# Optimization experiments

Hardware: AMD Instinct MI355X
Metric: run time of the kernel (lower is better)

The kernel has to match this reference:

```python
import jax, jax.numpy as jnp
import numpy as np

B, H, E, G, SEQ_LEN = 131072, 64, 16, 32, 30


def setup_inputs() -> dict:
    key = jax.random.key(0)
    ks = jax.random.split(key, 17)
    def lin(kw, kb, out_f, in_f):
        s = 1.0 / np.sqrt(in_f)
        W = jax.random.uniform(kw, (out_f, in_f), jnp.float32, -s, s)
        b = jax.random.uniform(kb, (out_f,), jnp.float32, -s, s)
        return W, b
    W_se, b_se = lin(ks[0], ks[1], E, 2)
    W_h2p, b_h2p = lin(ks[2], ks[3], 2, 3 * H)
    W_goal, b_goal = lin(ks[4], ks[5], H, 2 * G)
    W_abs, b_abs = lin(ks[6], ks[7], H, 2)
    W_ih, b_ih = lin(ks[8], ks[9], 4 * H, E)
    W_hh, b_hh = lin(ks[10], ks[11], 4 * H, H)
    return {
        "traj_abs": jax.random.normal(ks[12], (1, B, 2), jnp.float32),
        "traj_rel": jax.random.normal(ks[13], (1, B, 2), jnp.float32),
        "h0": jax.random.normal(ks[14], (1, B, H), jnp.float32),
        "c0": jax.random.normal(ks[15], (1, B, H), jnp.float32),
        "goals": jax.random.normal(ks[16], (B, G, 2), jnp.float32),
        "W_ih": W_ih, "W_hh": W_hh, "b_ih": b_ih, "b_hh": b_hh,
        "W_se": W_se, "b_se": b_se,
        "W_h2p": W_h2p, "b_h2p": b_h2p,
        "W_goal": W_goal, "b_goal": b_goal,
        "W_abs": W_abs, "b_abs": b_abs,
    }


def reference(traj_abs, traj_rel, h0, c0, goals,
              W_ih, W_hh, b_ih, b_hh,
              W_se, b_se, W_h2p, b_h2p,
              W_goal, b_goal, W_abs, b_abs):
    b = traj_abs.shape[1]
    goal_emb = goals.reshape(b, -1) @ W_goal.T + b_goal            # (b, H)
    dec_in = jax.nn.leaky_relu(traj_rel[0] @ W_se.T + b_se)        # (b, E)

    def step(carry, _):
        h, c, x, abs_pos = carry
        gates = x @ W_ih.T + b_ih + h @ W_hh.T + b_hh              # (b, 4H)
        i, f, g, o = jnp.split(gates, 4, axis=-1)                  # PyTorch gate order
        c = jax.nn.sigmoid(f) * c + jax.nn.sigmoid(i) * jnp.tanh(g)
        h = jax.nn.sigmoid(o) * jnp.tanh(c)
        abs_emb = abs_pos @ W_abs.T + b_abs                        # (b, H)
        inp = jnp.concatenate([h, abs_emb, goal_emb], axis=1)      # (b, 3H)
        rel = inp @ W_h2p.T + b_h2p                                # (b, 2)
        x = jax.nn.leaky_relu(rel @ W_se.T + b_se)
        return (h, c, x, abs_pos + rel), rel

    _, rels = jax.lax.scan(step, (h0[0], c0[0], dec_in, traj_abs[0]),
                           None, length=SEQ_LEN)
    return rels  # (seq_len, b, 2)
```

## Files before the change

### kernel.cpp

```cpp
#include <hip/hip_runtime.h>
#include <stdint.h>


#define B_TOT 131072
#define SEQL 30
#define NT 4

typedef _Float16 f16x8 __attribute__((ext_vector_type(8)));
typedef _Float16 f16x2 __attribute__((ext_vector_type(2)));
typedef float f32x4 __attribute__((ext_vector_type(4)));
typedef float f32x2 __attribute__((ext_vector_type(2)));

__device__ __forceinline__ float fexp2(float x) {
#if __has_builtin(__builtin_amdgcn_exp2f)
  return __builtin_amdgcn_exp2f(x);
#else
  return exp2f(x);
#endif
}
__device__ __forceinline__ float frcp(float x) {
#if __has_builtin(__builtin_amdgcn_rcpf)
  return __builtin_amdgcn_rcpf(x);
#else
  return 1.0f / x;
#endif
}

__global__ void setup_consts(const float* __restrict__ Wgoal,
                             const float* __restrict__ bgoal,
                             const float* __restrict__ Wh2p,
                             const float* __restrict__ bh2p,
                             const float* __restrict__ Wabs,
                             const float* __restrict__ babs,
                             float* __restrict__ wsf) {
  const int tid = threadIdx.x;
  const int wv = tid >> 6;
  const int lane = tid & 63;
  if (wv == 0) {
    const int k = lane;
    float s0 = 0.f, s1 = 0.f;
#pragma unroll 8
    for (int jj = 0; jj < 64; ++jj) {
      float wg = Wgoal[jj * 64 + k];
      s0 += wg * Wh2p[128 + jj];
      s1 += wg * Wh2p[320 + jj];
    }
    wsf[k] = s0;
    wsf[64 + k] = s1;
  } else {
    const int i = lane >> 3, sub = lane & 7;
    const int p = i & 1, grp = i >> 1;
    float s = 0.f;
#pragma unroll
    for (int t = 0; t < 8; ++t) {
      int j = sub * 8 + t;
      float wv_ = (grp < 3) ? Wh2p[p * 192 + 64 + j] : Wh2p[p * 192 + 128 + j];
      float av = (grp == 0)   ? Wabs[j * 2 + 0]
                 : (grp == 1) ? Wabs[j * 2 + 1]
                 : (grp == 2) ? babs[j]
                              : bgoal[j];
      s += av * wv_;
    }
    s += __shfl_xor(s, 1, 64);
    s += __shfl_xor(s, 2, 64);
    s += __shfl_xor(s, 4, 64);
    if (sub == 0) {
      if (grp == 2) s += bh2p[p];
      wsf[128 + i] = s;
    }
  }
}

__global__ __launch_bounds__(512, 4) void lstm_mfma(
    const float* __restrict__ tabs, const float* __restrict__ trel,
    const float* __restrict__ h0, const float* __restrict__ c0,
    const float* __restrict__ goals, const float* __restrict__ Wih,
    const float* __restrict__ Whh, const float* __restrict__ bih,
    const float* __restrict__ bhh, const float* __restrict__ Wse,
    const float* __restrict__ bse, const float* __restrict__ Wh2p,
    const float* __restrict__ wsf, float* __restrict__ outp) {
  const int lane = threadIdx.x & 63;
  const int w = threadIdx.x >> 6;
  const int wsl = w & 3;
  const int tp = w >> 2;
  const int q = lane >> 4;
  const int n = lane & 15;
  const int pm = n & 3;
  const int hs = 16 * wsl;
  const int bbase = blockIdx.x * (16 * NT);

  __shared__ __align__(16) _Float16 whh[4 * 64 * 64];
  __shared__ __align__(16) _Float16 wx[4 * 64 * 32];
  __shared__ __align__(16) _Float16 hbuf[2 * NT * 16 * 64];

  const float SI = -1.4426950408889634f;
  const float SG = 2.8853900817779268f;

  for (int idx = threadIdx.x; idx < 4 * 64 * 64; idx += 512) {
    const int r = idx >> 6, k = idx & 63;
    const float sc = ((r >> 6) == 2) ? SG : SI;
    const int slot = (k >> 3) ^ (r & 7);
    whh[r * 64 + slot * 8 + (k & 7)] = (_Float16)(sc * Whh[r * 64 + k]);
  }
  if (threadIdx.x < 256) {
    const int r = threadIdx.x;
    const float sc = ((r >> 6) == 2) ? SG : SI;
    float bfold = 0.f, m20 = 0.f, m21 = 0.f;
#pragma unroll
    for (int k = 0; k < 16; ++k) {
      float wik = Wih[r * 16 + k];
      bfold += bse[k] * wik;
      m20 += Wse[k * 2 + 0] * wik;
      m21 += Wse[k * 2 + 1] * wik;
    }
    const float bias = sc * (bih[r] + bhh[r] + 0.505f * bfold);
#pragma unroll
    for (int kx = 0; kx < 32; ++kx) {
      float v;
      if (kx < 16)
        v = sc * Wih[r * 16 + kx];
      else if (kx == 16)
        v = bias;
      else if (kx == 17)
        v = sc * 0.505f * m20;
      else if (kx == 18)
        v = sc * 0.505f * m21;
      else
        v = 0.f;
      const int slot = (kx >> 3) ^ (r & 3);
      wx[r * 32 + slot * 8 + (kx & 7)] = (_Float16)v;
    }
  }

  f16x8 awp0, awp1;
#pragma unroll
  for (int j = 0; j < 8; ++j) {
    float v0 = (pm < 2) ? Wh2p[pm * 192 + q * 8 + j] : 0.f;
    float v1 = (pm < 2) ? Wh2p[pm * 192 + 32 + q * 8 + j] : 0.f;
    awp0[j] = (_Float16)v0;
    awp1[j] = (_Float16)v1;
  }
  const float Sx0 = wsf[128], Sx1 = wsf[129];
  const float Sy0 = wsf[130], Sy1 = wsf[131];

  f16x2 wsaP[4], wsbP[4], bscP[4];
  const uint32_t xmask = (q < 2) ? 0x7FFF7FFFu : 0xFFFFFFFFu;
#pragma unroll
  for (int jj = 0; jj < 4; ++jj) {
    f16x2 z = f16x2{(_Float16)0.f, (_Float16)0.f};
    if (q < 2) {
      int kx = q * 8 + 2 * jj;
      wsaP[jj] = f16x2{(_Float16)(0.495f * Wse[kx * 2 + 0]),
                       (_Float16)(0.495f * Wse[kx * 2 + 2])};
      wsbP[jj] = f16x2{(_Float16)(0.495f * Wse[kx * 2 + 1]),
                       (_Float16)(0.495f * Wse[kx * 2 + 3])};
      bscP[jj] = f16x2{(_Float16)(0.495f * bse[kx]),
                       (_Float16)(0.495f * bse[kx + 1])};
    } else if (q == 2 && jj == 0) {
      wsaP[jj] = f16x2{(_Float16)0.f, (_Float16)1.f};
      wsbP[jj] = z;
      bscP[jj] = f16x2{(_Float16)1.f, (_Float16)0.f};
    } else if (q == 2 && jj == 1) {
      wsaP[jj] = z;
      wsbP[jj] = f16x2{(_Float16)1.f, (_Float16)0.f};
      bscP[jj] = z;
    } else {
      wsaP[jj] = z;
      wsbP[jj] = z;
      bscP[jj] = z;
    }
  }

  auto build_x = [&](float r0f, float r1f) -> f16x8 {
    f16x2 r0h = f16x2{(_Float16)r0f, (_Float16)r0f};
    f16x2 r1h = f16x2{(_Float16)r1f, (_Float16)r1f};
    f16x8 xr;
#pragma unroll
    for (int jj = 0; jj < 4; ++jj) {
      f16x2 t = r0h * wsaP[jj] + (r1h * wsbP[jj] + bscP[jj]);
      uint32_t tu = __builtin_bit_cast(uint32_t, t) & xmask;
      f16x2 lr = __builtin_bit_cast(f16x2, tu);
      xr[2 * jj] = lr[0];
      xr[2 * jj + 1] = lr[1];
    }
    return xr;
  };

  const f32x4 zC = {0.f, 0.f, 0.f, 0.f};

  float Gg0[2], Gg1[2];
  float ax[2], ay[2], cst[2][4];
  f16x8 xf[2];
  {
    f16x8 aM0, aM1;
#pragma unroll
    for (int j = 0; j < 8; ++j) {
      int k = q * 8 + j;
      aM0[j] = (_Float16)((pm < 2) ? wsf[pm * 64 + k] : 0.f);
      aM1[j] = (_Float16)((pm < 2) ? wsf[pm * 64 + 32 + k] : 0.f);
    }
    const float Sb0 = wsf[132] + wsf[134];
    const float Sb1 = wsf[133] + wsf[135];
#pragma unroll
    for (int u = 0; u < 2; ++u) {
      const int tg = 2 * tp + u;
      const int bb = bbase + 16 * tg;
      f16x8 bg0, bg1;
#pragma unroll
      for (int j = 0; j < 8; ++j) {
        int k = q * 8 + j;
        bg0[j] = (_Float16)goals[(bb + n) * 64 + k];
        bg1[j] = (_Float16)goals[(bb + n) * 64 + 32 + k];
      }
      f32x4 Ga = __builtin_amdgcn_mfma_f32_16x16x32_f16(aM0, bg0, zC, 0, 0, 0);
      Ga = __builtin_amdgcn_mfma_f32_16x16x32_f16(aM1, bg1, Ga, 0, 0, 0);
      Gg0[u] = Ga[0] + Sb0;
      Gg1[u] = Ga[1] + Sb1;

      ax[u] = tabs[(bb + n) * 2 + 0];
      ay[u] = tabs[(bb + n) * 2 + 1];
      const int cslot = (hs + n) >> 3, cin = n & 7;
#pragma unroll
      for (int r = 0; r < 4; ++r) {
        const int row = 4 * q + r;
        const int b = bb + row;
        cst[u][r] = c0[b * 64 + hs + n];
        hbuf[tg * 1024 + row * 64 + ((cslot ^ (row & 7)) << 3) + cin] =
            (_Float16)h0[b * 64 + hs + n];
      }
      xf[u] = build_x(trel[(bb + n) * 2 + 0], trel[(bb + n) * 2 + 1]);
    }
  }

  const int ro0 = n * 64 + ((q ^ (n & 7)) << 3);
  const int ro1 = n * 64 + (((4 + q) ^ (n & 7)) << 3);
  const int hb = (hs + n) * 64;
  const int sl0 = (q ^ (n & 7)) << 3;
  const int sl1 = (((4 + q) ^ (n & 7))) << 3;
  const int xb = (hs + n) * 32 + ((q ^ (n & 3)) << 3);
  const int wslot = (hs + n) >> 3, wcin = n & 7;

  const float K2 = 2.8853900817779268f;

  int poff = 0;
  for (int s = 0; s <= SEQL; ++s) {
    __syncthreads();
    f16x8 ah0[2], ah1[2];
#pragma unroll
    for (int u = 0; u < 2; ++u) {
      const int tb = poff + (2 * tp + u) * 1024;
      ah0[u] = *(const f16x8*)(hbuf + tb + ro0);
      ah1[u] = *(const f16x8*)(hbuf + tb + ro1);
    }

    if (s > 0) {
#pragma unroll
      for (int u = 0; u < 2; ++u) {
        f32x4 p = __builtin_amdgcn_mfma_f32_16x16x32_f16(awp0, ah0[u], zC,
                                                         0, 0, 0);
        p = __builtin_amdgcn_mfma_f32_16x16x32_f16(awp1, ah1[u], p, 0, 0, 0);
        float u0 = p[0] + Gg0[u] + fmaf(ax[u], Sx0, ay[u] * Sy0);
        float u1 = p[1] + Gg1[u] + fmaf(ax[u], Sx1, ay[u] * Sy1);
        ax[u] += u0;
        ay[u] += u1;
        if (wsl == u && lane < 16) {
          float2 v;
          v.x = u0;
          v.y = u1;
          ((float2*)outp)[(size_t)(s - 1) * B_TOT + bbase + 16 * (2 * tp + u) +
                          lane] = v;
        }
        xf[u] = build_x(u0, u1);
      }
    }

    if (s < SEQL) {
      f32x4 acc[2][4];
#pragma unroll
      for (int g = 0; g < 4; ++g) {
        const f16x8 w0 = *(const f16x8*)(whh + g * 4096 + hb + sl0);
        const f16x8 w1 = *(const f16x8*)(whh + g * 4096 + hb + sl1);
        const f16x8 w2 = *(const f16x8*)(wx + g * 2048 + xb);
#pragma unroll
        for (int u = 0; u < 2; ++u) {
          f32x4 a = __builtin_amdgcn_mfma_f32_16x16x32_f16(ah0[u], w0, zC,
                                                           0, 0, 0);
          a = __builtin_amdgcn_mfma_f32_16x16x32_f16(ah1[u], w1, a, 0, 0, 0);
          a = __builtin_amdgcn_mfma_f32_16x16x32_f16(xf[u], w2, a, 0, 0, 0);
          acc[u][g] = a;
        }
      }
#pragma unroll
      for (int u = 0; u < 2; ++u) {
        _Float16* hw = hbuf + (poff ^ 4096) + (2 * tp + u) * 1024;
#pragma unroll
        for (int pr = 0; pr < 2; ++pr) {
          const int ra = 2 * pr, rb = 2 * pr + 1;
          f32x2 Av = {fexp2(acc[u][0][ra]), fexp2(acc[u][0][rb])};
          f32x2 Fv = {fexp2(acc[u][1][ra]), fexp2(acc[u][1][rb])};
          f32x2 Bv = {fexp2(acc[u][2][ra]), fexp2(acc[u][2][rb])};
          const f32x2 one = {1.f, 1.f};
          f32x2 t1 = Av + one;
          f32x2 t2 = Bv + one;
          f32x2 t3 = Fv + one;
          f32x2 t4 = Bv - one;
          f32x2 m1 = t1 * t2;
          f32x2 cs = {cst[u][ra], cst[u][rb]};
          f32x2 num = cs * m1 + t4 * t3;
          f32x2 den = m1 * t3;
          float Rc = frcp(den[0] * den[1]);
          float cc0 = num[0] * den[1] * Rc;
          float cc1 = num[1] * den[0] * Rc;
          cst[u][ra] = cc0;
          cst[u][rb] = cc1;
          f32x2 Cv = {fexp2(acc[u][3][ra]), fexp2(acc[u][3][rb])};
          f32x2 Dv = {fexp2(K2 * cc0), fexp2(K2 * cc1)};
          f32x2 hd = (Cv + one) * (Dv + one);
          f32x2 hnm = Dv - one;
          float Rh = frcp(hd[0] * hd[1]);
          float h0v = hnm[0] * hd[1] * Rh;
          float h1v = hnm[1] * hd[0] * Rh;
          const int rowa = 4 * q + ra, rowb = 4 * q + rb;
          hw[rowa * 64 + ((wslot ^ (rowa & 7)) << 3) + wcin] = (_Float16)h0v;
          hw[rowb * 64 + ((wslot ^ (rowb & 7)) << 3) + wcin] = (_Float16)h1v;
        }
      }
      poff ^= 4096;
    }
  }
}

extern "C" void kernel_launch(void* const* d_in, const int* in_sizes, int n_in,
                              void* d_out, int out_size, void* d_ws,
                              size_t ws_size, hipStream_t stream) {
  (void)in_sizes; (void)n_in; (void)out_size; (void)ws_size;
  const float* tabs  = (const float*)d_in[0];
  const float* trel  = (const float*)d_in[1];
  const float* h0    = (const float*)d_in[2];
  const float* c0    = (const float*)d_in[3];
  const float* goals = (const float*)d_in[4];
  const float* Wih   = (const float*)d_in[5];
  const float* Whh   = (const float*)d_in[6];
  const float* bih   = (const float*)d_in[7];
  const float* bhh   = (const float*)d_in[8];
  const float* Wse   = (const float*)d_in[9];
  const float* bse   = (const float*)d_in[10];
  const float* Wh2p  = (const float*)d_in[11];
  const float* bh2p  = (const float*)d_in[12];
  const float* Wgoal = (const float*)d_in[13];
  const float* bgoal = (const float*)d_in[14];
  const float* Wabs  = (const float*)d_in[15];
  const float* babs  = (const float*)d_in[16];
  float* wsf = (float*)d_ws;

  setup_consts<<<dim3(1), dim3(128), 0, stream>>>(Wgoal, bgoal, Wh2p, bh2p,
                                                  Wabs, babs, wsf);
  lstm_mfma<<<dim3(B_TOT / (16 * NT)), dim3(512), 0, stream>>>(
      tabs, trel, h0, c0, goals, Wih, Whh, bih, bhh, Wse, bse, Wh2p, wsf,
      (float*)d_out);
}
```

Baseline: 468.9 us.

## Give each wave a whole batch tile to drop per-step block barriers

Before, eight waves split the 64 hidden units of each 16-row batch tile between them, so every step swapped h through a double-buffered LDS array and hit a block-wide __syncthreads. Now each wave owns one 16-row batch tile and computes all four 16-column hidden chunks itself. The recurrent h stays in a wave-private LDS scratch, so the per-step block barrier and the double buffer go away. Each block now covers 128 batch rows, which halves the grid. In exchange each wave holds more state (cell state for all 64 columns) and runs a longer serial chain of MFMA and transcendental work per step, which may raise register pressure.

```diff
diff --git a/kernel.cpp b/kernel.cpp
--- a/kernel.cpp
+++ b/kernel.cpp
@@ -4,7 +4,7 @@
 
 #define B_TOT 131072
 #define SEQL 30
-#define NT 4
+#define WPB 8
 
 typedef _Float16 f16x8 __attribute__((ext_vector_type(8)));
 typedef _Float16 f16x2 __attribute__((ext_vector_type(2)));
@@ -81,17 +81,14 @@
     const float* __restrict__ wsf, float* __restrict__ outp) {
   const int lane = threadIdx.x & 63;
   const int w = threadIdx.x >> 6;
-  const int wsl = w & 3;
-  const int tp = w >> 2;
   const int q = lane >> 4;
   const int n = lane & 15;
   const int pm = n & 3;
-  const int hs = 16 * wsl;
-  const int bbase = blockIdx.x * (16 * NT);
+  const int bb = blockIdx.x * (16 * WPB) + 16 * w;
 
   __shared__ __align__(16) _Float16 whh[4 * 64 * 64];
   __shared__ __align__(16) _Float16 wx[4 * 64 * 32];
-  __shared__ __align__(16) _Float16 hbuf[2 * NT * 16 * 64];
+  __shared__ __align__(16) _Float16 hscr[WPB * 16 * 64];
 
   const float SI = -1.4426950408889634f;
   const float SG = 2.8853900817779268f;
@@ -187,145 +184,123 @@
   };
 
   const f32x4 zC = {0.f, 0.f, 0.f, 0.f};
-
-  float Gg0[2], Gg1[2];
-  float ax[2], ay[2], cst[2][4];
-  f16x8 xf[2];
+  const int wbase = w * 1024;
+
+  float Gg0, Gg1, ax, ay;
+  float cst[4][4];
+  f16x8 xf;
   {
-    f16x8 aM0, aM1;
+    f16x8 aM0, aM1, bg0, bg1;
 #pragma unroll
     for (int j = 0; j < 8; ++j) {
       int k = q * 8 + j;
       aM0[j] = (_Float16)((pm < 2) ? wsf[pm * 64 + k] : 0.f);
       aM1[j] = (_Float16)((pm < 2) ? wsf[pm * 64 + 32 + k] : 0.f);
-    }
-    const float Sb0 = wsf[132] + wsf[134];
-    const float Sb1 = wsf[133] + wsf[135];
-#pragma unroll
-    for (int u = 0; u < 2; ++u) {
-      const int tg = 2 * tp + u;
-      const int bb = bbase + 16 * tg;
-      f16x8 bg0, bg1;
-#pragma unroll
-      for (int j = 0; j < 8; ++j) {
-        int k = q * 8 + j;
-        bg0[j] = (_Float16)goals[(bb + n) * 64 + k];
-        bg1[j] = (_Float16)goals[(bb + n) * 64 + 32 + k];
+      bg0[j] = (_Float16)goals[(bb + n) * 64 + k];
+      bg1[j] = (_Float16)goals[(bb + n) * 64 + 32 + k];
+    }
+    f32x4 Ga = __builtin_amdgcn_mfma_f32_16x16x32_f16(aM0, bg0, zC, 0, 0, 0);
+    Ga = __builtin_amdgcn_mfma_f32_16x16x32_f16(aM1, bg1, Ga, 0, 0, 0);
+    Gg0 = Ga[0] + wsf[132] + wsf[134];
+    Gg1 = Ga[1] + wsf[133] + wsf[135];
+
+    ax = tabs[(bb + n) * 2 + 0];
+    ay = tabs[(bb + n) * 2 + 1];
+#pragma unroll
+    for (int m = 0; m < 4; ++m) {
+      const int c16 = 2 * m + (n >> 3);
+#pragma unroll
+      for (int r = 0; r < 4; ++r) {
+        const int br = 4 * q + r;
+        cst[m][r] = c0[(bb + br) * 64 + 16 * m + n];
+        hscr[wbase + br * 64 + ((c16 ^ (br & 7)) << 3) + (n & 7)] =
+            (_Float16)h0[(bb + br) * 64 + 16 * m + n];
       }
-      f32x4 Ga = __builtin_amdgcn_mfma_f32_16x16x32_f16(aM0, bg0, zC, 0, 0, 0);
-      Ga = __builtin_amdgcn_mfma_f32_16x16x32_f16(aM1, bg1, Ga, 0, 0, 0);
-      Gg0[u] = Ga[0] + Sb0;
-      Gg1[u] = Ga[1] + Sb1;
-
-      ax[u] = tabs[(bb + n) * 2 + 0];
-      ay[u] = tabs[(bb + n) * 2 + 1];
-      const int cslot = (hs + n) >> 3, cin = n & 7;
-#pragma unroll
-      for (int r = 0; r < 4; ++r) {
-        const int row = 4 * q + r;
-        const int b = bb + row;
-        cst[u][r] = c0[b * 64 + hs + n];
-        hbuf[tg * 1024 + row * 64 + ((cslot ^ (row & 7)) << 3) + cin] =
-            (_Float16)h0[b * 64 + hs + n];
+    }
+    xf = build_x(trel[(bb + n) * 2 + 0], trel[(bb + n) * 2 + 1]);
+  }
+
+  __syncthreads();
+
+  const int ro0 = wbase + n * 64 + ((q ^ (n & 7)) << 3);
+  const int ro1 = wbase + n * 64 + (((4 + q) ^ (n & 7)) << 3);
+  const int sl0 = (q ^ (n & 7)) << 3;
+  const int sl1 = ((4 + q) ^ (n & 7)) << 3;
+  const int xsl = (q ^ (n & 3)) << 3;
+  const float K2 = 2.8853900817779268f;
+
+  for (int s = 0; s <= SEQL; ++s) {
+    const f16x8 ah0 = *(const f16x8*)(hscr + ro0);
+    const f16x8 ah1 = *(const f16x8*)(hscr + ro1);
+
+    if (s > 0) {
+      f32x4 p = __builtin_amdgcn_mfma_f32_16x16x32_f16(awp0, ah0, zC, 0, 0, 0);
+      p = __builtin_amdgcn_mfma_f32_16x16x32_f16(awp1, ah1, p, 0, 0, 0);
+      float u0 = p[0] + Gg0 + fmaf(ax, Sx0, ay * Sy0);
+      float u1 = p[1] + Gg1 + fmaf(ax, Sx1, ay * Sy1);
+      ax += u0;
+      ay += u1;
+      if (lane < 16) {
+        float2 v;
+        v.x = u0;
+        v.y = u1;
+        ((float2*)outp)[(size_t)(s - 1) * B_TOT + bb + lane] = v;
       }
-      xf[u] = build_x(trel[(bb + n) * 2 + 0], trel[(bb + n) * 2 + 1]);
-    }
-  }
-
-  const int ro0 = n * 64 + ((q ^ (n & 7)) << 3);
-  const int ro1 = n * 64 + (((4 + q) ^ (n & 7)) << 3);
-  const int hb = (hs + n) * 64;
-  const int sl0 = (q ^ (n & 7)) << 3;
-  const int sl1 = (((4 + q) ^ (n & 7))) << 3;
-  const int xb = (hs + n) * 32 + ((q ^ (n & 3)) << 3);
-  const int wslot = (hs + n) >> 3, wcin = n & 7;
-
-  const float K2 = 2.8853900817779268f;
-
-  int poff = 0;
-  for (int s = 0; s <= SEQL; ++s) {
-    __syncthreads();
-    f16x8 ah0[2], ah1[2];
-#pragma unroll
-    for (int u = 0; u < 2; ++u) {
-      const int tb = poff + (2 * tp + u) * 1024;
-      ah0[u] = *(const f16x8*)(hbuf + tb + ro0);
-      ah1[u] = *(const f16x8*)(hbuf + tb + ro1);
-    }
-
-    if (s > 0) {
-#pragma unroll
-      for (int u = 0; u < 2; ++u) {
-        f32x4 p = __builtin_amdgcn_mfma_f32_16x16x32_f16(awp0, ah0[u], zC,
-                                                         0, 0, 0);
-        p = __builtin_amdgcn_mfma_f32_16x16x32_f16(awp1, ah1[u], p, 0, 0, 0);
-        float u0 = p[0] + Gg0[u] + fmaf(ax[u], Sx0, ay[u] * Sy0);
-        float u1 = p[1] + Gg1[u] + fmaf(ax[u], Sx1, ay[u] * Sy1);
-        ax[u] += u0;
-        ay[u] += u1;
-        if (wsl == u && lane < 16) {
-          float2 v;
-          v.x = u0;
-          v.y = u1;
-          ((float2*)outp)[(size_t)(s - 1) * B_TOT + bbase + 16 * (2 * tp + u) +
-                          lane] = v;
+      xf = build_x(u0, u1);
+    }
+
+    if (s < SEQL) {
+#pragma unroll
+      for (int m = 0; m < 4; ++m) {
+        const int hb = (16 * m + n) * 64;
+        const int xb = (16 * m + n) * 32 + xsl;
+        f32x4 acc[4];
+#pragma unroll
+        for (int g = 0; g < 4; ++g) {
+          const f16x8 w0 = *(const f16x8*)(whh + g * 4096 + hb + sl0);
+          const f16x8 w1 = *(const f16x8*)(whh + g * 4096 + hb + sl1);
+          const f16x8 w2 = *(const f16x8*)(wx + g * 2048 + xb);
+          f32x4 a = __builtin_amdgcn_mfma_f32_16x16x32_f16(ah0, w0, zC,
+                                                           0, 0, 0);
+          a = __builtin_amdgcn_mfma_f32_16x16x32_f16(ah1, w1, a, 0, 0, 0);
+          a = __builtin_amdgcn_mfma_f32_16x16x32_f16(xf, w2, a, 0, 0, 0);
+          acc[g] = a;
         }
-        xf[u] = build_x(u0, u1);
-      }
-    }
-
-    if (s < SEQL) {
-      f32x4 acc[2][4];
-#pragma unroll
-      for (int g = 0; g < 4; ++g) {
-        const f16x8 w0 = *(const f16x8*)(whh + g * 4096 + hb + sl0);
-        const f16x8 w1 = *(const f16x8*)(whh + g * 4096 + hb + sl1);
-        const f16x8 w2 = *(const f16x8*)(wx + g * 2048 + xb);
-#pragma unroll
-        for (int u = 0; u < 2; ++u) {
-          f32x4 a = __builtin_amdgcn_mfma_f32_16x16x32_f16(ah0[u], w0, zC,
-                                                           0, 0, 0);
-          a = __builtin_amdgcn_mfma_f32_16x16x32_f16(ah1[u], w1, a, 0, 0, 0);
-          a = __builtin_amdgcn_mfma_f32_16x16x32_f16(xf[u], w2, a, 0, 0, 0);
-          acc[u][g] = a;
-        }
-      }
-#pragma unroll
-      for (int u = 0; u < 2; ++u) {
-        _Float16* hw = hbuf + (poff ^ 4096) + (2 * tp + u) * 1024;
+        const int c16 = 2 * m + (n >> 3);
 #pragma unroll
         for (int pr = 0; pr < 2; ++pr) {
           const int ra = 2 * pr, rb = 2 * pr + 1;
-          f32x2 Av = {fexp2(acc[u][0][ra]), fexp2(acc[u][0][rb])};
-          f32x2 Fv = {fexp2(acc[u][1][ra]), fexp2(acc[u][1][rb])};
-          f32x2 Bv = {fexp2(acc[u][2][ra]), fexp2(acc[u][2][rb])};
+          f32x2 Av = {fexp2(acc[0][ra]), fexp2(acc[0][rb])};
+          f32x2 Fv = {fexp2(acc[1][ra]), fexp2(acc[1][rb])};
+          f32x2 Bv = {fexp2(acc[2][ra]), fexp2(acc[2][rb])};
           const f32x2 one = {1.f, 1.f};
           f32x2 t1 = Av + one;
           f32x2 t2 = Bv + one;
           f32x2 t3 = Fv + one;
           f32x2 t4 = Bv - one;
           f32x2 m1 = t1 * t2;
-          f32x2 cs = {cst[u][ra], cst[u][rb]};
+          f32x2 cs = {cst[m][ra], cst[m][rb]};
           f32x2 num = cs * m1 + t4 * t3;
           f32x2 den = m1 * t3;
           float Rc = frcp(den[0] * den[1]);
           float cc0 = num[0] * den[1] * Rc;
           float cc1 = num[1] * den[0] * Rc;
-          cst[u][ra] = cc0;
-          cst[u][rb] = cc1;
-          f32x2 Cv = {fexp2(acc[u][3][ra]), fexp2(acc[u][3][rb])};
+          cst[m][ra] = cc0;
+          cst[m][rb] = cc1;
+          f32x2 Cv = {fexp2(acc[3][ra]), fexp2(acc[3][rb])};
           f32x2 Dv = {fexp2(K2 * cc0), fexp2(K2 * cc1)};
           f32x2 hd = (Cv + one) * (Dv + one);
           f32x2 hnm = Dv - one;
           float Rh = frcp(hd[0] * hd[1]);
           float h0v = hnm[0] * hd[1] * Rh;
           float h1v = hnm[1] * hd[0] * Rh;
-          const int rowa = 4 * q + ra, rowb = 4 * q + rb;
-          hw[rowa * 64 + ((wslot ^ (rowa & 7)) << 3) + wcin] = (_Float16)h0v;
-          hw[rowb * 64 + ((wslot ^ (rowb & 7)) << 3) + wcin] = (_Float16)h1v;
+          const int bra = 4 * q + ra, brb = 4 * q + rb;
+          hscr[wbase + bra * 64 + ((c16 ^ (bra & 7)) << 3) + (n & 7)] =
+              (_Float16)h0v;
+          hscr[wbase + brb * 64 + ((c16 ^ (brb & 7)) << 3) + (n & 7)] =
+              (_Float16)h1v;
         }
       }
-      poff ^= 4096;
     }
   }
 }
@@ -355,7 +330,7 @@
 
   setup_consts<<<dim3(1), dim3(128), 0, stream>>>(Wgoal, bgoal, Wh2p, bh2p,
                                                   Wabs, babs, wsf);
-  lstm_mfma<<<dim3(B_TOT / (16 * NT)), dim3(512), 0, stream>>>(
+  lstm_mfma<<<dim3(B_TOT / (16 * WPB)), dim3(512), 0, stream>>>(
       tabs, trel, h0, c0, goals, Wih, Whh, bih, bhh, Wse, bse, Wh2p, wsf,
       (float*)d_out);
 }
```

New measurement: 447.4 us. -4.6%, faster.
